# Kernel tuning notes

Hardware: AMD Instinct MI355X
Metric: run time of the kernel (lower is better)

## Reference

```python
import jax, jax.numpy as jnp
import numpy as np

HEADS = 8
DIM_HEAD = 64
EPS = 1e-5  # fp32 eps in ChanLayerNorm


def chan_layer_norm(x, g):
    # x: [b, c, h, w]; normalize over channel dim with biased variance
    mean = jnp.mean(x, axis=1, keepdims=True)
    var = jnp.var(x, axis=1, keepdims=True)
    return (x - mean) * jax.lax.rsqrt(var + EPS) * g[None, :, None, None]


def setup_inputs() -> dict:
    key = jax.random.key(0)
    k1, k2, k3 = jax.random.split(key, 3)
    dim, inner = 512, HEADS * DIM_HEAD
    fmap = jax.random.normal(k1, (16, dim, 64, 64), dtype=jnp.float32)
    # 1x1 conv weights (no bias); scaled like typical init to keep softmax unsaturated
    w_qkv = jax.random.normal(k2, (3 * inner, dim), dtype=jnp.float32) * 0.02
    w_out = jax.random.normal(k3, (dim, inner), dtype=jnp.float32) * 0.02
    g1 = jnp.ones((dim,), dtype=jnp.float32)
    g2 = jnp.ones((dim,), dtype=jnp.float32)
    return {"fmap": fmap, "g1": g1, "w_qkv": w_qkv, "w_out": w_out, "g2": g2}


def reference(fmap, g1, w_qkv, w_out, g2):
    b, c, X, Y = fmap.shape
    h, dh = HEADS, DIM_HEAD
    n = X * Y  # seq_len
    scale = dh ** -0.5

    x = chan_layer_norm(fmap, g1)
    # 1x1 conv == channel matmul: [b, 3*inner, X, Y]
    qkv = jnp.einsum('bcxy,oc->boxy', x, w_qkv)
    q, k, v = jnp.split(qkv, 3, axis=1)

    def to_bhnc(t):
        # b (h c) x y -> b h n c
        return t.reshape(b, h, dh, n).transpose(0, 1, 3, 2)

    q, k, v = map(to_bhnc, (q, k, v))

    q = jax.nn.softmax(q, axis=-1) * scale          # softmax over feature dim
    k = jax.nn.softmax(k, axis=2)                   # softmax over seq dim
    v = v / jnp.linalg.norm(v, axis=-1, keepdims=True)  # l2norm
    inv_sqrt_n = 1.0 / np.sqrt(n)
    k = k * inv_sqrt_n
    v = v * inv_sqrt_n

    context = jnp.einsum('bhnd,bhne->bhde', k, v)   # small d x e context
    out = jnp.einsum('bhnd,bhde->bhne', q, context)  # [b, h, n, dh]

    # b h n d -> b (h d) x y
    out = out.transpose(0, 1, 3, 2).reshape(b, h * dh, X, Y)
    out = jax.nn.gelu(out, approximate=False)
    out = jnp.einsum('bcxy,oc->boxy', out, w_out)
    return chan_layer_norm(out, g2)
```

## Files before the change

### kernel.cpp

```cpp
#include <hip/hip_runtime.h>

typedef unsigned short u16;
typedef __attribute__((ext_vector_type(2))) float f32x2;
typedef __attribute__((ext_vector_type(4))) float f32x4;
typedef __attribute__((ext_vector_type(8))) short s16x8;
typedef __attribute__((ext_vector_type(8))) u16 u16x8;
typedef __attribute__((ext_vector_type(4))) u16 u16x4;

#define NB 16
#define CD 512
#define NS 4096
#define NHD 8

#define SBAR  __builtin_amdgcn_s_barrier()
#define SCHED __builtin_amdgcn_sched_barrier(0)
#define PRIO1 __builtin_amdgcn_s_setprio(1)
#define PRIO0 __builtin_amdgcn_s_setprio(0)

__device__ __forceinline__ float bf2f(u16 u){
  union { unsigned int i; float f; } z; z.i = ((unsigned int)u) << 16; return z.f;
}
__device__ __forceinline__ u16 f2bf(float f){
  union { float f; unsigned int i; } z; z.f = f;
  unsigned int i = z.i;
  return (u16)((i + 0x7fffu + ((i >> 16) & 1u)) >> 16);
}
__device__ __forceinline__ float gelu_f(float x){
  return 0.5f * x * (1.0f + erff(x * 0.70710678118654752440f));
}
__device__ __forceinline__ void gl_lds16(const u16* g, u16* l){
  __builtin_amdgcn_global_load_lds((const __attribute__((address_space(1))) void*)(g),
                                   (__attribute__((address_space(3))) void*)(l), 16, 0, 0);
}

__global__ void prep_w_k(const float* __restrict__ wqkv, const float* __restrict__ g1,
                         const float* __restrict__ wout, u16* __restrict__ w1b,
                         u16* __restrict__ w2b){
  int i = blockIdx.x * 256 + threadIdx.x;
  if (i < 1536*512) {
    w1b[i] = f2bf(wqkv[i] * g1[i & 511]);
  } else {
    int j = i - 1536*512;
    w2b[j] = f2bf(wout[j]);
  }
}

__global__ __launch_bounds__(512) void ln1t_k(const float* __restrict__ fmap,
                                              u16* __restrict__ xlnT){
  int b = blockIdx.y, n0 = blockIdx.x * 32;
  int t = threadIdx.x;
  int lane = t & 63, wv = t >> 6;
  __shared__ u16 Lb[512][40];
  __shared__ u16 Tt[64][36];
  __shared__ float red1[8][8][4], red2[8][8][4];
  __shared__ float mean_s[32], rstd_s[32];

  int ng = t & 7;
  float s1[4] = {0,0,0,0}, s2[4] = {0,0,0,0};
  const float* fb = fmap + ((size_t)b*CD)*NS + n0 + ng*4;
  #pragma unroll
  for (int it = 0; it < 8; ++it){
    int q = it*512 + t;
    int c = q >> 3;
    f32x4 v = *(const f32x4*)&fb[(size_t)c*NS];
    u16x4 pk;
    #pragma unroll
    for (int j = 0; j < 4; ++j){
      pk[j] = f2bf(v[j]);
      s1[j] += v[j]; s2[j] += v[j]*v[j];
    }
    *(u16x4*)&Lb[c][ng*4] = pk;
  }
  #pragma unroll
  for (int off = 8; off < 64; off <<= 1)
    #pragma unroll
    for (int j = 0; j < 4; ++j){
      s1[j] += __shfl_xor(s1[j], off, 64);
      s2[j] += __shfl_xor(s2[j], off, 64);
    }
  if (lane < 8){
    #pragma unroll
    for (int j = 0; j < 4; ++j){ red1[wv][lane][j] = s1[j]; red2[wv][lane][j] = s2[j]; }
  }
  __syncthreads();
  if (t < 32){
    int g = t >> 2, j = t & 3;
    float a = 0.f, bq = 0.f;
    #pragma unroll
    for (int w = 0; w < 8; ++w){ a += red1[w][g][j]; bq += red2[w][g][j]; }
    float mn = a * (1.f/512.f);
    float var = bq * (1.f/512.f) - mn*mn;
    mean_s[t] = mn; rstd_s[t] = rsqrtf(var + 1e-5f);
  }
  __syncthreads();

  for (int ct = 0; ct < 8; ++ct){
    {
      int cl = t >> 3, n4 = (t & 7) * 4;
      u16x4 xv = *(const u16x4*)&Lb[ct*64 + cl][n4];
      u16x4 pk;
      #pragma unroll
      for (int j = 0; j < 4; ++j)
        pk[j] = f2bf((bf2f(xv[j]) - mean_s[n4+j]) * rstd_s[n4+j]);
      *(u16x4*)&Tt[cl][n4] = pk;
    }
    __syncthreads();
    {
      int nr = t >> 4, c4 = t & 15;
      u16x4 w;
      #pragma unroll
      for (int j = 0; j < 4; ++j) w[j] = Tt[c4*4 + j][nr];
      *(u16x4*)&xlnT[((size_t)b*NS + n0 + nr)*CD + ct*64 + c4*4] = w;
    }
    __syncthreads();
  }
}

__global__ __launch_bounds__(512) void gemm1_k(const u16* __restrict__ A,
                                               const u16* __restrict__ Bm,
                                               u16* __restrict__ Cm){
  __shared__ u16 lds[2][4][8192];
  int bi = blockIdx.x;
  int xcd = bi & 7, r2 = bi >> 3;
  int gi = r2 / 6, yy = r2 - gi*6;
  int g  = gi*8 + xcd;
  int x  = g & 15, z = g >> 4;
  int o0 = yy*256, bn0 = x*256;
  int t = threadIdx.x;
  int lane = t & 63, wv = t >> 6;
  int wm = wv >> 2, wn = wv & 3;
  int fr = lane & 15, fg = lane >> 4;
  const u16* Ab = A + (size_t)o0*512;
  const u16* Bb = Bm + ((size_t)z*NS + bn0)*512;
  int li8 = lane >> 3, scn = lane & 7;

  f32x4 acc[8][4];
  #pragma unroll
  for (int i=0;i<8;++i)
    #pragma unroll
    for (int j=0;j<4;++j) acc[i][j] = (f32x4){0.f,0.f,0.f,0.f};
  s16x8 afr[4][2];
  s16x8 bfr[2][2][2];

  auto stH = [&](int slot, int half, int kt){
    #pragma unroll
    for (int it=0; it<2; ++it){
      int li = it*64 + wv*8 + li8;
      int q  = scn ^ (li & 7);
      int row;
      if (half < 2) row = ((li>>6)<<7) + half*64 + (li & 63);
      else          row = ((li>>5)<<6) + (half-2)*32 + (li & 31);
      const u16* G = (half < 2) ? Ab : Bb;
      gl_lds16(G + (size_t)row*512 + kt + q*8, &lds[slot][half][it*4096 + wv*512]);
    }
  };
  auto ldA = [&](int slot, int mq){
    #pragma unroll
    for (int mr=0;mr<4;++mr)
      #pragma unroll
      for (int ks=0;ks<2;++ks){
        int li = wm*64 + mr*16 + fr;
        int c8 = (ks*4+fg) ^ (li & 7);
        afr[mr][ks] = *(const s16x8*)&lds[slot][mq][li*64 + c8*8];
      }
  };
  auto ldB = [&](int slot, int nq){
    #pragma unroll
    for (int nr=0;nr<2;++nr)
      #pragma unroll
      for (int ks=0;ks<2;++ks){
        int li = wn*32 + nr*16 + fr;
        int c8 = (ks*4+fg) ^ (li & 7);
        bfr[nq][nr][ks] = *(const s16x8*)&lds[slot][2+nq][li*64 + c8*8];
      }
  };
  auto mm = [&](int mq, int nq){
    #pragma unroll
    for (int mr=0;mr<4;++mr)
      #pragma unroll
      for (int nr=0;nr<2;++nr)
        #pragma unroll
        for (int ks=0;ks<2;++ks)
          acc[mq*4+mr][nq*2+nr] = __builtin_amdgcn_mfma_f32_16x16x32_bf16(
              afr[mr][ks], bfr[nq][nr][ks], acc[mq*4+mr][nq*2+nr], 0,0,0);
  };

  stH(0,0,0); stH(0,2,0); stH(0,3,0); stH(0,1,0);
  asm volatile("s_waitcnt vmcnt(2)" ::: "memory");
  SBAR; SCHED;

  #pragma unroll
  for (int kt=0; kt<8; ++kt){
    int slot = kt & 1, ns = slot ^ 1, kn = (kt+1)*64;
    bool F = kt < 7;
    ldA(slot,0); ldB(slot,0); ldB(slot,1);
    if (F){ stH(ns,0,kn); stH(ns,2,kn); stH(ns,3,kn); }
    PRIO1; mm(0,0); mm(0,1); PRIO0;
    if (F) asm volatile("s_waitcnt vmcnt(6)" ::: "memory");
    else   asm volatile("s_waitcnt vmcnt(0)" ::: "memory");
    SBAR; SCHED;
    ldA(slot,1);
    if (F) stH(ns,1,kn);
    PRIO1; mm(1,1); mm(1,0); PRIO0;
    if (F) asm volatile("s_waitcnt vmcnt(2)" ::: "memory");
    SBAR; SCHED;
  }

  size_t cb = (size_t)z * 1536 * NS;
  #pragma unroll
  for (int mq=0;mq<2;++mq)
    #pragma unroll
    for (int mr=0;mr<4;++mr)
      #pragma unroll
      for (int nq=0;nq<2;++nq)
        #pragma unroll
        for (int nr=0;nr<2;++nr){
          int row = o0 + wm*128 + mq*64 + mr*16 + fg*4;
          int col = bn0 + wn*64 + nq*32 + nr*16 + fr;
          #pragma unroll
          for (int r=0;r<4;++r)
            Cm[cb + (size_t)(row+r)*NS + col] = f2bf(acc[mq*4+mr][nq*2+nr][r]);
        }
}

__global__ __launch_bounds__(512) void gemm2f_k(const u16* __restrict__ A,
                                                const u16* __restrict__ qkv,
                                                const float* __restrict__ ctx,
                                                const float* __restrict__ g2,
                                                float* __restrict__ out){
  __shared__ u16 Ar[2][16384];
  __shared__ u16 Bh[2][4096];
  __shared__ u16 P[128][72];
  __shared__ u16 cT[64][72];
  __shared__ float invP[128];
  int x = blockIdx.x, z = blockIdx.y;
  int n0 = x*128;
  int t = threadIdx.x;
  int lane = t & 63, wv = t >> 6;
  int wm = wv >> 1, wn = wv & 1;
  int wn2 = wv >> 2, we = wv & 3;
  int fr = lane & 15, fg = lane >> 4;
  int l8 = lane >> 3, c8d = lane & 7;
  const u16* Ab = A;

  f32x4 acc[8][4];
  #pragma unroll
  for (int i=0;i<8;++i)
    #pragma unroll
    for (int j=0;j<4;++j) acc[i][j] = (f32x4){0.f,0.f,0.f,0.f};
  s16x8 afr[4], bfr[4];

  auto stA4 = [&](int slot, int kt){
    #pragma unroll
    for (int bt=0; bt<4; ++bt){
      int L  = bt*64 + wv*8 + l8;
      int q  = c8d ^ (l8 & 7);
      int r  = (q >> 2)*256 + L;
      int col = kt + (q & 3)*8;
      gl_lds16(Ab + (size_t)r*512 + col, &Ar[slot][(bt*64 + wv*8)*64]);
    }
  };
  auto ldA = [&](int slot, int h2){
    #pragma unroll
    for (int mi=0;mi<4;++mi){
      int R = wm*128 + (h2*4+mi)*16 + fr;
      int L = R & 255, half = R >> 8;
      int c8 = (half*4 + fg) ^ (L & 7);
      afr[mi] = *(const s16x8*)&Ar[slot][L*64 + c8*8];
    }
  };
  auto ldBh = [&](int kt2){
    #pragma unroll
    for (int nj=0;nj<4;++nj){
      int R = wn*64 + nj*16 + fr;
      int L = R & 63, half = R >> 6;
      int c8 = (half*4 + fg) ^ (L & 7);
      bfr[nj] = *(const s16x8*)&Bh[kt2][L*64 + c8*8];
    }
  };
  auto mm16 = [&](int h2){
    #pragma unroll
    for (int mi=0;mi<4;++mi)
      #pragma unroll
      for (int nj=0;nj<4;++nj)
        acc[h2*4+mi][nj] = __builtin_amdgcn_mfma_f32_16x16x32_bf16(
            afr[mi], bfr[nj], acc[h2*4+mi][nj], 0,0,0);
  };

  stA4(0, 0);

  for (int h = 0; h < 8; ++h){
    const float* cs = ctx + ((size_t)(z*8 + h))*4096;
    #pragma unroll
    for (int i=0;i<8;++i){
      int idx = i*512 + t;
      cT[idx & 63][idx >> 6] = f2bf(cs[idx]);
    }
    {
      int nl = wv*16 + (lane & 15);
      int dg = lane >> 4;
      const u16* qb = qkv + ((size_t)(z*1536 + h*64 + dg*16))*NS + n0 + nl;
      float p[16];
      float m = -3.0e38f;
      #pragma unroll
      for (int j=0;j<16;++j){ p[j] = bf2f(qb[(size_t)j*NS]); m = fmaxf(m, p[j]); }
      m = fmaxf(m, __shfl_xor(m, 16, 64));
      m = fmaxf(m, __shfl_xor(m, 32, 64));
      float s = 0.f;
      #pragma unroll
      for (int j=0;j<16;++j){ p[j] = __expf(p[j]-m); s += p[j]; }
      s += __shfl_xor(s, 16, 64);
      s += __shfl_xor(s, 32, 64);
      u16x8 pk;
      #pragma unroll
      for (int j=0;j<8;++j) pk[j] = f2bf(p[j]);
      *(u16x8*)&P[nl][dg*16] = pk;
      #pragma unroll
      for (int j=0;j<8;++j) pk[j] = f2bf(p[8+j]);
      *(u16x8*)&P[nl][dg*16+8] = pk;
      if (dg == 0) invP[nl] = 0.125f / s;
    }
    __syncthreads();
    stA4(1, (2*h+1)*32);

    f32x4 a2[4];
    #pragma unroll
    for (int i=0;i<4;++i) a2[i] = (f32x4){0.f,0.f,0.f,0.f};
    #pragma unroll
    for (int ks=0; ks<2; ++ks){
      s16x8 bfx = *(const s16x8*)&cT[we*16 + fr][ks*32 + fg*8];
      #pragma unroll
      for (int nf=0; nf<4; ++nf){
        s16x8 afx = *(const s16x8*)&P[wn2*64 + nf*16 + fr][ks*32 + fg*8];
        a2[nf] = __builtin_amdgcn_mfma_f32_16x16x32_bf16(afx, bfx, a2[nf], 0,0,0);
      }
    }
    {
      int kt2w = we >> 1;
      #pragma unroll
      for (int nf=0; nf<4; ++nf)
        #pragma unroll
        for (int r=0; r<4; ++r){
          int nl2 = wn2*64 + nf*16 + fg*4 + r;
          int e = we*16 + fr;
          int col = e & 31;
          int L = nl2 & 63;
          int c8 = ((nl2>>6)*4 + (col>>3)) ^ (L & 7);
          Bh[kt2w][L*64 + c8*8 + (col&7)] = f2bf(gelu_f(a2[nf][r] * invP[nl2]));
        }
    }
    asm volatile("s_waitcnt vmcnt(4)" ::: "memory");
    __syncthreads();
    ldA(0,0); ldBh(0);
    PRIO1; mm16(0); PRIO0;
    ldA(0,1);
    PRIO1; mm16(1); PRIO0;
    asm volatile("s_waitcnt vmcnt(0)" ::: "memory");
    __syncthreads();
    if (h < 7) stA4(0, (2*h+2)*32);
    ldA(1,0); ldBh(1);
    PRIO1; mm16(0); PRIO0;
    ldA(1,1);
    PRIO1; mm16(1); PRIO0;
  }

  __syncthreads();
  float* red1 = (float*)&Ar[0][0];
  float* red2 = red1 + 512;
  float* ms   = red2 + 512;
  float* rs   = ms + 128;
  float s1[4], s2[4];
  #pragma unroll
  for (int nj=0;nj<4;++nj){
    float a = 0.f, b2 = 0.f;
    #pragma unroll
    for (int mi=0;mi<8;++mi)
      #pragma unroll
      for (int r=0;r<4;++r){ float v = acc[mi][nj][r]; a += v; b2 += v*v; }
    s1[nj] = a; s2[nj] = b2;
  }
  #pragma unroll
  for (int off=16; off<64; off<<=1)
    #pragma unroll
    for (int nj=0;nj<4;++nj){
      s1[nj] += __shfl_xor(s1[nj], off, 64);
      s2[nj] += __shfl_xor(s2[nj], off, 64);
    }
  if (fg == 0){
    #pragma unroll
    for (int nj=0;nj<4;++nj){
      int c = wn*64 + nj*16 + fr;
      red1[wm*128 + c] = s1[nj];
      red2[wm*128 + c] = s2[nj];
    }
  }
  __syncthreads();
  if (t < 128){
    float a  = red1[t] + red1[128+t] + red1[256+t] + red1[384+t];
    float b2 = red2[t] + red2[128+t] + red2[256+t] + red2[384+t];
    float mn = a * (1.f/512.f);
    float var = b2 * (1.f/512.f) - mn*mn;
    ms[t] = mn; rs[t] = rsqrtf(var + 1e-5f);
  }
  __syncthreads();
  float mc[4], rc[4];
  #pragma unroll
  for (int nj=0;nj<4;++nj){
    int c = wn*64 + nj*16 + fr;
    mc[nj] = ms[c]; rc[nj] = rs[c];
  }
  float* ob = out + (size_t)z*CD*NS + n0;
  #pragma unroll
  for (int mi=0;mi<8;++mi)
    #pragma unroll
    for (int r=0;r<4;++r){
      int row = wm*128 + mi*16 + fg*4 + r;
      float gg = g2[row];
      #pragma unroll
      for (int nj=0;nj<4;++nj)
        ob[(size_t)row*NS + wn*64 + nj*16 + fr] = (acc[mi][nj][r] - mc[nj])*rc[nj]*gg;
    }
}

__global__ __launch_bounds__(256) void ctxpart_k(const u16* __restrict__ qkv,
                                                 float* __restrict__ part,
                                                 float* __restrict__ mS){
  int chunk = blockIdx.x, bh = blockIdx.y;
  int b = bh >> 3, h = bh & 7;
  int t = threadIdx.x;
  int lane = t & 63, wv = t >> 6;
  int fr = lane & 15, fg = lane >> 4;
  __shared__ u16 KT[64*128];
  __shared__ u16 VT[64*128];
  __shared__ float invn_s[128];
  const u16* kb = qkv + ((size_t)(b*1536 + 512  + h*64))*NS;
  const u16* vb = qkv + ((size_t)(b*1536 + 1024 + h*64))*NS;
  int d = t >> 2, q = t & 3;

  float sloc = 0.f;

  f32x4 acc[4][4];
  #pragma unroll
  for (int i=0;i<4;++i)
    #pragma unroll
    for (int j=0;j<4;++j) acc[i][j] = (f32x4){0.f,0.f,0.f,0.f};

  for (int nt = 0; nt < 4; ++nt){
    int n0 = chunk*512 + nt*128;
    if (nt) __syncthreads();
    u16x8 kreg[4];
    #pragma unroll
    for (int s = 0; s < 4; ++s){
      int c0 = q*32 + s*8;
      u16x8 vv = *(const u16x8*)&vb[(size_t)d*NS + n0 + c0];
      *(u16x8*)&VT[d*128 + (c0 ^ ((d&7)<<3))] = vv;
      kreg[s] = *(const u16x8*)&kb[(size_t)d*NS + n0 + c0];
    }
    __syncthreads();
    {
      int col = t >> 1, half = t & 1;
      float ss = 0.f;
      #pragma unroll
      for (int e2 = 0; e2 < 32; ++e2){
        int e = half*32 + e2;
        float xv = bf2f(VT[e*128 + (col ^ ((e&7)<<3))]);
        ss += xv*xv;
      }
      ss += __shfl_xor(ss, 1, 64);
      if (half == 0) invn_s[col] = rsqrtf(ss);
    }
    __syncthreads();
    #pragma unroll
    for (int s = 0; s < 4; ++s){
      int c0 = q*32 + s*8;
      u16x8 kk = kreg[s];
      u16x8 ek;
      #pragma unroll
      for (int j = 0; j < 8; ++j){
        float e = __expf(bf2f(kk[j]));
        sloc += e;
        ek[j] = f2bf(e * invn_s[c0 + j]);
      }
      *(u16x8*)&KT[d*128 + (c0 ^ ((d&7)<<3))] = ek;
    }
    __syncthreads();
    int kc = wv*32 + fg*8;
    s16x8 af[4], bfr[4];
    #pragma unroll
    for (int i=0;i<4;++i){
      int ra = i*16 + fr;
      af[i]  = *(const s16x8*)&KT[ra*128 + (kc ^ ((ra&7)<<3))];
      bfr[i] = *(const s16x8*)&VT[ra*128 + (kc ^ ((ra&7)<<3))];
    }
    #pragma unroll
    for (int i=0;i<4;++i)
      #pragma unroll
      for (int j=0;j<4;++j)
        acc[i][j] = __builtin_amdgcn_mfma_f32_16x16x32_bf16(af[i], bfr[j], acc[i][j], 0,0,0);
  }

  sloc += __shfl_xor(sloc, 1, 64);
  sloc += __shfl_xor(sloc, 2, 64);
  if (q == 0){
    size_t mb = ((size_t)bh*8 + chunk)*128;
    mS[mb + d]      = 0.0f;
    mS[mb + 64 + d] = sloc;
  }

  float* buf0 = (float*)KT;
  float* buf1 = (float*)VT;
  auto dump = [&](float* bf){
    #pragma unroll
    for (int i=0;i<4;++i)
      #pragma unroll
      for (int j=0;j<4;++j)
        #pragma unroll
        for (int r=0;r<4;++r) bf[((i*4+j)*4+r)*64 + lane] = acc[i][j][r];
  };
  auto addin = [&](float* bf){
    #pragma unroll
    for (int i=0;i<4;++i)
      #pragma unroll
      for (int j=0;j<4;++j)
        #pragma unroll
        for (int r=0;r<4;++r) acc[i][j][r] += bf[((i*4+j)*4+r)*64 + lane];
  };
  __syncthreads();
  if (wv==1) dump(buf0);
  if (wv==3) dump(buf1);
  __syncthreads();
  if (wv==0) addin(buf0);
  if (wv==2) addin(buf1);
  __syncthreads();
  if (wv==2) dump(buf0);
  __syncthreads();
  if (wv==0){
    addin(buf0);
    float* pp = part + ((size_t)bh*8 + chunk)*4096;
    #pragma unroll
    for (int i=0;i<4;++i)
      #pragma unroll
      for (int j=0;j<4;++j)
        #pragma unroll
        for (int r=0;r<4;++r)
          pp[(i*16+fg*4+r)*64 + j*16+fr] = acc[i][j][r];
  }
}

__global__ void ctxred_k(const float* __restrict__ part, const float* __restrict__ mS,
                         float* __restrict__ ctx){
  int bh = blockIdx.x, t = threadIdx.x;
  __shared__ float fs[8][64];
  if (t < 64){
    int d = t;
    float mc[8];
    float mx = -3.0e38f;
    #pragma unroll
    for (int c=0;c<8;++c){ mc[c] = mS[((size_t)bh*8 + c)*128 + d]; mx = fmaxf(mx, mc[c]); }
    float es[8]; float denom = 0.f;
    #pragma unroll
    for (int c=0;c<8;++c){
      es[c] = __expf(mc[c] - mx);
      denom += es[c] * mS[((size_t)bh*8 + c)*128 + 64 + d];
    }
    float inv = 1.0f / (denom * 4096.0f);
    #pragma unroll
    for (int c=0;c<8;++c) fs[c][d] = es[c] * inv;
  }
  __syncthreads();
  #pragma unroll
  for (int i=0;i<16;++i){
    int idx = t + i*256;
    int d = idx >> 6;
    float s = 0.f;
    #pragma unroll
    for (int ch=0; ch<8; ++ch) s += fs[ch][d] * part[((size_t)bh*8 + ch)*4096 + idx];
    ctx[(size_t)bh*4096 + idx] = s;
  }
}

extern "C" void kernel_launch(void* const* d_in, const int* in_sizes, int n_in,
                              void* d_out, int out_size, void* d_ws, size_t ws_size,
                              hipStream_t stream) {
  const float* fmap = (const float*)d_in[0];
  const float* g1   = (const float*)d_in[1];
  const float* wqkv = (const float*)d_in[2];
  const float* wout = (const float*)d_in[3];
  const float* g2   = (const float*)d_in[4];
  float* out = (float*)d_out;

  char* ws = (char*)d_ws;
  size_t off = 0;
  auto alloc = [&](size_t bytes) -> void* {
    void* p = ws + off;
    off += (bytes + 255) & ~(size_t)255;
    return p;
  };
  u16*   qkv  = (u16*)alloc((size_t)16*1536*4096*2);
  u16*   xlnT = (u16*)alloc((size_t)16*4096*512*2);
  float* part = (float*)alloc((size_t)128*8*4096*4);
  float* mS   = (float*)alloc((size_t)128*8*128*4);
  float* ctx  = (float*)alloc((size_t)128*4096*4);
  u16*   w1b  = (u16*)alloc((size_t)1536*512*2);
  u16*   w2b  = (u16*)alloc((size_t)512*512*2);
  if (off > ws_size) return;

  prep_w_k<<<4096, 256, 0, stream>>>(wqkv, g1, wout, w1b, w2b);
  ln1t_k<<<dim3(128,16), 512, 0, stream>>>(fmap, xlnT);
  gemm1_k<<<1536, 512, 0, stream>>>(w1b, xlnT, qkv);
  ctxpart_k<<<dim3(8,128), 256, 0, stream>>>(qkv, part, mS);
  ctxred_k<<<128, 256, 0, stream>>>(part, mS, ctx);
  gemm2f_k<<<dim3(32,16), 512, 0, stream>>>(w2b, qkv, ctx, g2, out);
}
```

Measured before the change: 308.9 us.

## Fuse K/V projection with context accumulation, materialize only Q

Splits the QKV projection GEMM into a Q-only GEMM and a K/V GEMM. The K/V GEMM applies exp and the V l2-normalisation in its epilogue and computes the partial K^T V context per 256-column tile directly from shared memory, so K and V never go to global memory and the separate ctxpart kernel is removed. The exp is taken without max subtraction, which relies on K values being small, and the partial-context buffer doubles to 16 chunks per head, so the reduction kernel reads more partials.

New measurement: 287.5 us. 6.9% less time.

```diff
diff --git a/kernel.cpp b/kernel.cpp
--- a/kernel.cpp
+++ b/kernel.cpp
@@ -116,13 +116,13 @@
   }
 }
 
-__global__ __launch_bounds__(512) void gemm1_k(const u16* __restrict__ A,
-                                               const u16* __restrict__ Bm,
-                                               u16* __restrict__ Cm){
-  __shared__ u16 lds[2][4][8192];
+__global__ __launch_bounds__(512) void gemm1q_k(const u16* __restrict__ A,
+                                                const u16* __restrict__ Bm,
+                                                u16* __restrict__ Q){
+  __shared__ u16 lds[8][8192];
   int bi = blockIdx.x;
   int xcd = bi & 7, r2 = bi >> 3;
-  int gi = r2 / 6, yy = r2 - gi*6;
+  int yy = r2 & 1, gi = r2 >> 1;
   int g  = gi*8 + xcd;
   int x  = g & 15, z = g >> 4;
   int o0 = yy*256, bn0 = x*256;
@@ -151,7 +151,7 @@
       if (half < 2) row = ((li>>6)<<7) + half*64 + (li & 63);
       else          row = ((li>>5)<<6) + (half-2)*32 + (li & 31);
       const u16* G = (half < 2) ? Ab : Bb;
-      gl_lds16(G + (size_t)row*512 + kt + q*8, &lds[slot][half][it*4096 + wv*512]);
+      gl_lds16(G + (size_t)row*512 + kt + q*8, &lds[slot*4+half][it*4096 + wv*512]);
     }
   };
   auto ldA = [&](int slot, int mq){
@@ -161,7 +161,7 @@
       for (int ks=0;ks<2;++ks){
         int li = wm*64 + mr*16 + fr;
         int c8 = (ks*4+fg) ^ (li & 7);
-        afr[mr][ks] = *(const s16x8*)&lds[slot][mq][li*64 + c8*8];
+        afr[mr][ks] = *(const s16x8*)&lds[slot*4+mq][li*64 + c8*8];
       }
   };
   auto ldB = [&](int slot, int nq){
@@ -171,7 +171,7 @@
       for (int ks=0;ks<2;++ks){
         int li = wn*32 + nr*16 + fr;
         int c8 = (ks*4+fg) ^ (li & 7);
-        bfr[nq][nr][ks] = *(const s16x8*)&lds[slot][2+nq][li*64 + c8*8];
+        bfr[nq][nr][ks] = *(const s16x8*)&lds[slot*4+2+nq][li*64 + c8*8];
       }
   };
   auto mm = [&](int mq, int nq){
@@ -206,7 +206,7 @@
     SBAR; SCHED;
   }
 
-  size_t cb = (size_t)z * 1536 * NS;
+  size_t cb = (size_t)z * 512 * NS;
   #pragma unroll
   for (int mq=0;mq<2;++mq)
     #pragma unroll
@@ -219,12 +219,261 @@
           int col = bn0 + wn*64 + nq*32 + nr*16 + fr;
           #pragma unroll
           for (int r=0;r<4;++r)
-            Cm[cb + (size_t)(row+r)*NS + col] = f2bf(acc[mq*4+mr][nq*2+nr][r]);
+            Q[cb + (size_t)(row+r)*NS + col] = f2bf(acc[mq*4+mr][nq*2+nr][r]);
         }
 }
 
+__global__ __launch_bounds__(512) void gemm1kv_k(const u16* __restrict__ A,
+                                                 const u16* __restrict__ Bm,
+                                                 float* __restrict__ part,
+                                                 float* __restrict__ mS){
+  __shared__ u16 lds[8][8192];
+  int bi = blockIdx.x;
+  int xcd = bi & 7, r2 = bi >> 3;
+  int hp = r2 & 3, gg = r2 >> 2;
+  int g8 = gg*8 + xcd;
+  int x  = g8 & 15, z = g8 >> 4;
+  int bn0 = x*256;
+  int t = threadIdx.x;
+  int lane = t & 63, wv = t >> 6;
+  int wm = wv >> 2, wn = wv & 3;
+  int fr = lane & 15, fg = lane >> 4;
+  const u16* Akb = A + (size_t)(512  + hp*128)*512;
+  const u16* Avb = A + (size_t)(1024 + hp*128)*512;
+  const u16* Bb  = Bm + ((size_t)z*NS + bn0)*512;
+  int li8 = lane >> 3, scn = lane & 7;
+
+  f32x4 acc[8][4];
+  #pragma unroll
+  for (int i=0;i<8;++i)
+    #pragma unroll
+    for (int j=0;j<4;++j) acc[i][j] = (f32x4){0.f,0.f,0.f,0.f};
+  s16x8 afr[4][2];
+  s16x8 bfr[2][2][2];
+
+  auto stH = [&](int slot, int half, int kt){
+    #pragma unroll
+    for (int it=0; it<2; ++it){
+      int li = it*64 + wv*8 + li8;
+      int q  = scn ^ (li & 7);
+      if (half < 2){
+        int rr = half*64 + (li & 63);
+        const u16* G = it ? Avb : Akb;
+        gl_lds16(G + (size_t)rr*512 + kt + q*8, &lds[slot*4+half][it*4096 + wv*512]);
+      } else {
+        int row = ((li>>5)<<6) + (half-2)*32 + (li & 31);
+        gl_lds16(Bb + (size_t)row*512 + kt + q*8, &lds[slot*4+half][it*4096 + wv*512]);
+      }
+    }
+  };
+  auto ldA = [&](int slot, int mq){
+    #pragma unroll
+    for (int mr=0;mr<4;++mr)
+      #pragma unroll
+      for (int ks=0;ks<2;++ks){
+        int li = wm*64 + mr*16 + fr;
+        int c8 = (ks*4+fg) ^ (li & 7);
+        afr[mr][ks] = *(const s16x8*)&lds[slot*4+mq][li*64 + c8*8];
+      }
+  };
+  auto ldB = [&](int slot, int nq){
+    #pragma unroll
+    for (int nr=0;nr<2;++nr)
+      #pragma unroll
+      for (int ks=0;ks<2;++ks){
+        int li = wn*32 + nr*16 + fr;
+        int c8 = (ks*4+fg) ^ (li & 7);
+        bfr[nq][nr][ks] = *(const s16x8*)&lds[slot*4+2+nq][li*64 + c8*8];
+      }
+  };
+  auto mm = [&](int mq, int nq){
+    #pragma unroll
+    for (int mr=0;mr<4;++mr)
+      #pragma unroll
+      for (int nr=0;nr<2;++nr)
+        #pragma unroll
+        for (int ks=0;ks<2;++ks)
+          acc[mq*4+mr][nq*2+nr] = __builtin_amdgcn_mfma_f32_16x16x32_bf16(
+              afr[mr][ks], bfr[nq][nr][ks], acc[mq*4+mr][nq*2+nr], 0,0,0);
+  };
+
+  stH(0,0,0); stH(0,2,0); stH(0,3,0); stH(0,1,0);
+  asm volatile("s_waitcnt vmcnt(2)" ::: "memory");
+  SBAR; SCHED;
+
+  #pragma unroll
+  for (int kt=0; kt<8; ++kt){
+    int slot = kt & 1, ns = slot ^ 1, kn = (kt+1)*64;
+    bool F = kt < 7;
+    ldA(slot,0); ldB(slot,0); ldB(slot,1);
+    if (F){ stH(ns,0,kn); stH(ns,2,kn); stH(ns,3,kn); }
+    PRIO1; mm(0,0); mm(0,1); PRIO0;
+    if (F) asm volatile("s_waitcnt vmcnt(6)" ::: "memory");
+    else   asm volatile("s_waitcnt vmcnt(0)" ::: "memory");
+    SBAR; SCHED;
+    ldA(slot,1);
+    if (F) stH(ns,1,kn);
+    PRIO1; mm(1,1); mm(1,0); PRIO0;
+    if (F) asm volatile("s_waitcnt vmcnt(2)" ::: "memory");
+    SBAR; SCHED;
+  }
+
+  if (wm == 0){
+    #pragma unroll
+    for (int mq=0;mq<2;++mq)
+      #pragma unroll
+      for (int mr=0;mr<4;++mr)
+        #pragma unroll
+        for (int nj=0;nj<4;++nj){
+          int nq = nj>>1, nr = nj&1;
+          #pragma unroll
+          for (int r=0;r<4;++r){
+            int d  = mr*16 + fg*4 + r;
+            int nl = wn*64 + nq*32 + nr*16 + fr;
+            int hh = nl >> 7, n1 = nl & 127;
+            lds[mq*2+hh][d*128 + (n1 ^ ((d&7)<<3))] = f2bf(__expf(acc[mq*4+mr][nj][r]));
+          }
+        }
+  } else {
+    float ss[2][4];
+    #pragma unroll
+    for (int mq=0;mq<2;++mq)
+      #pragma unroll
+      for (int nj=0;nj<4;++nj){
+        float s = 0.f;
+        #pragma unroll
+        for (int mr=0;mr<4;++mr)
+          #pragma unroll
+          for (int r=0;r<4;++r){ float v = acc[mq*4+mr][nj][r]; s += v*v; }
+        s += __shfl_xor(s, 16, 64);
+        s += __shfl_xor(s, 32, 64);
+        ss[mq][nj] = rsqrtf(s);
+      }
+    #pragma unroll
+    for (int mq=0;mq<2;++mq)
+      #pragma unroll
+      for (int mr=0;mr<4;++mr)
+        #pragma unroll
+        for (int nj=0;nj<4;++nj){
+          int nq = nj>>1, nr = nj&1;
+          #pragma unroll
+          for (int r=0;r<4;++r){
+            int e  = mr*16 + fg*4 + r;
+            int nl = wn*64 + nq*32 + nr*16 + fr;
+            int hh = nl >> 7, n1 = nl & 127;
+            lds[4 + mq*2+hh][e*128 + (n1 ^ ((e&7)<<3))] = f2bf(acc[mq*4+mr][nj][r] * ss[mq][nj]);
+          }
+        }
+  }
+  __syncthreads();
+
+  int eg = wv >> 2, ej = wv & 3, ksl = ej & 1;
+  const u16* KTt = &lds[eg*2 + (ej>>1)][0];
+  const u16* VTt = &lds[4 + eg*2 + (ej>>1)][0];
+  f32x4 a2[4][4];
+  #pragma unroll
+  for (int i=0;i<4;++i)
+    #pragma unroll
+    for (int j=0;j<4;++j) a2[i][j] = (f32x4){0.f,0.f,0.f,0.f};
+  #pragma unroll
+  for (int ks2=0; ks2<2; ++ks2){
+    int kc = ksl*64 + ks2*32 + fg*8;
+    s16x8 af[4], bf_[4];
+    #pragma unroll
+    for (int i=0;i<4;++i){
+      int ra = i*16 + fr;
+      af[i]  = *(const s16x8*)&KTt[ra*128 + (kc ^ ((ra&7)<<3))];
+      bf_[i] = *(const s16x8*)&VTt[ra*128 + (kc ^ ((ra&7)<<3))];
+    }
+    #pragma unroll
+    for (int i=0;i<4;++i)
+      #pragma unroll
+      for (int j=0;j<4;++j)
+        a2[i][j] = __builtin_amdgcn_mfma_f32_16x16x32_bf16(af[i], bf_[j], a2[i][j], 0,0,0);
+  }
+  float slc = 0.f;
+  {
+    int d = lane;
+    #pragma unroll
+    for (int cc=0; cc<8; ++cc){
+      int c0 = ksl*64 + cc*8;
+      u16x8 vv = *(const u16x8*)&KTt[d*128 + (c0 ^ ((d&7)<<3))];
+      #pragma unroll
+      for (int jj=0;jj<8;++jj) slc += bf2f(vv[jj]);
+    }
+  }
+  __syncthreads();
+
+  if (ej >= 1){
+    float* dbuf = (float*)&lds[eg*3 + (ej-1)][0];
+    #pragma unroll
+    for (int i=0;i<4;++i)
+      #pragma unroll
+      for (int j=0;j<4;++j)
+        #pragma unroll
+        for (int r=0;r<4;++r) dbuf[((i*4+j)*4+r)*64 + lane] = a2[i][j][r];
+  }
+  ((float*)&lds[6][0])[eg*256 + ej*64 + lane] = slc;
+  __syncthreads();
+
+  int bh = z*8 + hp*2 + eg;
+  size_t base = (size_t)bh*16 + x;
+  if (ej == 0){
+    #pragma unroll
+    for (int bb=0; bb<3; ++bb){
+      float* dbuf = (float*)&lds[eg*3 + bb][0];
+      #pragma unroll
+      for (int i=0;i<4;++i)
+        #pragma unroll
+        for (int j=0;j<4;++j)
+          #pragma unroll
+          for (int r=0;r<4;++r) a2[i][j][r] += dbuf[((i*4+j)*4+r)*64 + lane];
+    }
+    float* pp = part + base*4096;
+    #pragma unroll
+    for (int i=0;i<4;++i)
+      #pragma unroll
+      for (int j=0;j<4;++j)
+        #pragma unroll
+        for (int r=0;r<4;++r)
+          pp[(i*16+fg*4+r)*64 + j*16+fr] = a2[i][j][r];
+  } else if (ej == 1){
+    float* sB = (float*)&lds[6][0];
+    float s = sB[eg*256 + lane] + sB[eg*256 + 64 + lane]
+            + sB[eg*256 + 128 + lane] + sB[eg*256 + 192 + lane];
+    mS[base*128 + lane]      = 0.0f;
+    mS[base*128 + 64 + lane] = s;
+  }
+}
+
+__global__ void ctxred_k(const float* __restrict__ part, const float* __restrict__ mS,
+                         float* __restrict__ ctx){
+  int bh = blockIdx.x, t = threadIdx.x;
+  __shared__ float fs[16][64];
+  if (t < 64){
+    int d = t;
+    float denom = 0.f;
+    #pragma unroll
+    for (int c=0;c<16;++c)
+      denom += mS[((size_t)bh*16 + c)*128 + 64 + d];
+    float inv = 1.0f / (denom * 4096.0f);
+    #pragma unroll
+    for (int c=0;c<16;++c) fs[c][d] = inv;
+  }
+  __syncthreads();
+  #pragma unroll
+  for (int i=0;i<16;++i){
+    int idx = t + i*256;
+    int d = idx >> 6;
+    float s = 0.f;
+    #pragma unroll
+    for (int ch=0; ch<16; ++ch) s += fs[ch][d] * part[((size_t)bh*16 + ch)*4096 + idx];
+    ctx[(size_t)bh*4096 + idx] = s;
+  }
+}
+
 __global__ __launch_bounds__(512) void gemm2f_k(const u16* __restrict__ A,
-                                                const u16* __restrict__ qkv,
+                                                const u16* __restrict__ q,
                                                 const float* __restrict__ ctx,
                                                 const float* __restrict__ g2,
                                                 float* __restrict__ out){
@@ -254,9 +503,9 @@
     #pragma unroll
     for (int bt=0; bt<4; ++bt){
       int L  = bt*64 + wv*8 + l8;
-      int q  = c8d ^ (l8 & 7);
-      int r  = (q >> 2)*256 + L;
-      int col = kt + (q & 3)*8;
+      int qq = c8d ^ (l8 & 7);
+      int r  = (qq >> 2)*256 + L;
+      int col = kt + (qq & 3)*8;
       gl_lds16(Ab + (size_t)r*512 + col, &Ar[slot][(bt*64 + wv*8)*64]);
     }
   };
@@ -299,7 +548,7 @@
     {
       int nl = wv*16 + (lane & 15);
       int dg = lane >> 4;
-      const u16* qb = qkv + ((size_t)(z*1536 + h*64 + dg*16))*NS + n0 + nl;
+      const u16* qb = q + ((size_t)(z*512 + h*64 + dg*16))*NS + n0 + nl;
       float p[16];
       float m = -3.0e38f;
       #pragma unroll
@@ -422,163 +671,6 @@
     }
 }
 
-__global__ __launch_bounds__(256) void ctxpart_k(const u16* __restrict__ qkv,
-                                                 float* __restrict__ part,
-                                                 float* __restrict__ mS){
-  int chunk = blockIdx.x, bh = blockIdx.y;
-  int b = bh >> 3, h = bh & 7;
-  int t = threadIdx.x;
-  int lane = t & 63, wv = t >> 6;
-  int fr = lane & 15, fg = lane >> 4;
-  __shared__ u16 KT[64*128];
-  __shared__ u16 VT[64*128];
-  __shared__ float invn_s[128];
-  const u16* kb = qkv + ((size_t)(b*1536 + 512  + h*64))*NS;
-  const u16* vb = qkv + ((size_t)(b*1536 + 1024 + h*64))*NS;
-  int d = t >> 2, q = t & 3;
-
-  float sloc = 0.f;
-
-  f32x4 acc[4][4];
-  #pragma unroll
-  for (int i=0;i<4;++i)
-    #pragma unroll
-    for (int j=0;j<4;++j) acc[i][j] = (f32x4){0.f,0.f,0.f,0.f};
-
-  for (int nt = 0; nt < 4; ++nt){
-    int n0 = chunk*512 + nt*128;
-    if (nt) __syncthreads();
-    u16x8 kreg[4];
-    #pragma unroll
-    for (int s = 0; s < 4; ++s){
-      int c0 = q*32 + s*8;
-      u16x8 vv = *(const u16x8*)&vb[(size_t)d*NS + n0 + c0];
-      *(u16x8*)&VT[d*128 + (c0 ^ ((d&7)<<3))] = vv;
-      kreg[s] = *(const u16x8*)&kb[(size_t)d*NS + n0 + c0];
-    }
-    __syncthreads();
-    {
-      int col = t >> 1, half = t & 1;
-      float ss = 0.f;
-      #pragma unroll
-      for (int e2 = 0; e2 < 32; ++e2){
-        int e = half*32 + e2;
-        float xv = bf2f(VT[e*128 + (col ^ ((e&7)<<3))]);
-        ss += xv*xv;
-      }
-      ss += __shfl_xor(ss, 1, 64);
-      if (half == 0) invn_s[col] = rsqrtf(ss);
-    }
-    __syncthreads();
-    #pragma unroll
-    for (int s = 0; s < 4; ++s){
-      int c0 = q*32 + s*8;
-      u16x8 kk = kreg[s];
-      u16x8 ek;
-      #pragma unroll
-      for (int j = 0; j < 8; ++j){
-        float e = __expf(bf2f(kk[j]));
-        sloc += e;
-        ek[j] = f2bf(e * invn_s[c0 + j]);
-      }
-      *(u16x8*)&KT[d*128 + (c0 ^ ((d&7)<<3))] = ek;
-    }
-    __syncthreads();
-    int kc = wv*32 + fg*8;
-    s16x8 af[4], bfr[4];
-    #pragma unroll
-    for (int i=0;i<4;++i){
-      int ra = i*16 + fr;
-      af[i]  = *(const s16x8*)&KT[ra*128 + (kc ^ ((ra&7)<<3))];
-      bfr[i] = *(const s16x8*)&VT[ra*128 + (kc ^ ((ra&7)<<3))];
-    }
-    #pragma unroll
-    for (int i=0;i<4;++i)
-      #pragma unroll
-      for (int j=0;j<4;++j)
-        acc[i][j] = __builtin_amdgcn_mfma_f32_16x16x32_bf16(af[i], bfr[j], acc[i][j], 0,0,0);
-  }
-
-  sloc += __shfl_xor(sloc, 1, 64);
-  sloc += __shfl_xor(sloc, 2, 64);
-  if (q == 0){
-    size_t mb = ((size_t)bh*8 + chunk)*128;
-    mS[mb + d]      = 0.0f;
-    mS[mb + 64 + d] = sloc;
-  }
-
-  float* buf0 = (float*)KT;
-  float* buf1 = (float*)VT;
-  auto dump = [&](float* bf){
-    #pragma unroll
-    for (int i=0;i<4;++i)
-      #pragma unroll
-      for (int j=0;j<4;++j)
-        #pragma unroll
-        for (int r=0;r<4;++r) bf[((i*4+j)*4+r)*64 + lane] = acc[i][j][r];
-  };
-  auto addin = [&](float* bf){
-    #pragma unroll
-    for (int i=0;i<4;++i)
-      #pragma unroll
-      for (int j=0;j<4;++j)
-        #pragma unroll
-        for (int r=0;r<4;++r) acc[i][j][r] += bf[((i*4+j)*4+r)*64 + lane];
-  };
-  __syncthreads();
-  if (wv==1) dump(buf0);
-  if (wv==3) dump(buf1);
-  __syncthreads();
-  if (wv==0) addin(buf0);
-  if (wv==2) addin(buf1);
-  __syncthreads();
-  if (wv==2) dump(buf0);
-  __syncthreads();
-  if (wv==0){
-    addin(buf0);
-    float* pp = part + ((size_t)bh*8 + chunk)*4096;
-    #pragma unroll
-    for (int i=0;i<4;++i)
-      #pragma unroll
-      for (int j=0;j<4;++j)
-        #pragma unroll
-        for (int r=0;r<4;++r)
-          pp[(i*16+fg*4+r)*64 + j*16+fr] = acc[i][j][r];
-  }
-}
-
-__global__ void ctxred_k(const float* __restrict__ part, const float* __restrict__ mS,
-                         float* __restrict__ ctx){
-  int bh = blockIdx.x, t = threadIdx.x;
-  __shared__ float fs[8][64];
-  if (t < 64){
-    int d = t;
-    float mc[8];
-    float mx = -3.0e38f;
-    #pragma unroll
-    for (int c=0;c<8;++c){ mc[c] = mS[((size_t)bh*8 + c)*128 + d]; mx = fmaxf(mx, mc[c]); }
-    float es[8]; float denom = 0.f;
-    #pragma unroll
-    for (int c=0;c<8;++c){
-      es[c] = __expf(mc[c] - mx);
-      denom += es[c] * mS[((size_t)bh*8 + c)*128 + 64 + d];
-    }
-    float inv = 1.0f / (denom * 4096.0f);
-    #pragma unroll
-    for (int c=0;c<8;++c) fs[c][d] = es[c] * inv;
-  }
-  __syncthreads();
-  #pragma unroll
-  for (int i=0;i<16;++i){
-    int idx = t + i*256;
-    int d = idx >> 6;
-    float s = 0.f;
-    #pragma unroll
-    for (int ch=0; ch<8; ++ch) s += fs[ch][d] * part[((size_t)bh*8 + ch)*4096 + idx];
-    ctx[(size_t)bh*4096 + idx] = s;
-  }
-}
-
 extern "C" void kernel_launch(void* const* d_in, const int* in_sizes, int n_in,
                               void* d_out, int out_size, void* d_ws, size_t ws_size,
                               hipStream_t stream) {
@@ -596,10 +688,10 @@
     off += (bytes + 255) & ~(size_t)255;
     return p;
   };
-  u16*   qkv  = (u16*)alloc((size_t)16*1536*4096*2);
+  u16*   q    = (u16*)alloc((size_t)16*512*4096*2);
   u16*   xlnT = (u16*)alloc((size_t)16*4096*512*2);
-  float* part = (float*)alloc((size_t)128*8*4096*4);
-  float* mS   = (float*)alloc((size_t)128*8*128*4);
+  float* part = (float*)alloc((size_t)128*16*4096*4);
+  float* mS   = (float*)alloc((size_t)128*16*128*4);
   float* ctx  = (float*)alloc((size_t)128*4096*4);
   u16*   w1b  = (u16*)alloc((size_t)1536*512*2);
   u16*   w2b  = (u16*)alloc((size_t)512*512*2);
@@ -607,8 +699,8 @@
 
   prep_w_k<<<4096, 256, 0, stream>>>(wqkv, g1, wout, w1b, w2b);
   ln1t_k<<<dim3(128,16), 512, 0, stream>>>(fmap, xlnT);
-  gemm1_k<<<1536, 512, 0, stream>>>(w1b, xlnT, qkv);
-  ctxpart_k<<<dim3(8,128), 256, 0, stream>>>(qkv, part, mS);
+  gemm1q_k<<<512, 512, 0, stream>>>(w1b, xlnT, q);
+  gemm1kv_k<<<1024, 512, 0, stream>>>(w1b, xlnT, part, mS);
   ctxred_k<<<128, 256, 0, stream>>>(part, mS, ctx);
-  gemm2f_k<<<dim3(32,16), 512, 0, stream>>>(w2b, qkv, ctx, g2, out);
-}
+  gemm2f_k<<<dim3(32,16), 512, 0, stream>>>(w2b, q, ctx, g2, out);
+}
```
